# Performance work log

Measured on AMD Instinct MI355X. Metric: run time of the kernel, lower is better.

Reference implementation:

```python
import jax, jax.numpy as jnp
import numpy as np

B, S, P, D = 32, 512, 512, 768

def setup_inputs() -> dict:
    key = jax.random.key(0)
    k1, k2 = jax.random.split(key)
    inputs = jax.random.normal(k1, (B, S, D), dtype=jnp.float32)
    prototypes = jax.random.normal(k2, (P, D), dtype=jnp.float32)
    return {"inputs": inputs, "prototypes": prototypes}

def reference(inputs, prototypes):
    # Squared Euclidean distance from every token vector to every prototype:
    # but the cross term is a GEMM and the huge [B,S,P,D] intermediate is never built).
    x_sq = jnp.sum(inputs * inputs, axis=-1, keepdims=True)          # [B, S, 1]
    p_sq = jnp.sum(prototypes * prototypes, axis=-1)                 # [P]
    cross = jnp.einsum('bsd,pd->bsp', inputs, prototypes)            # [B, S, P]
    distances = x_sq + p_sq[None, None, :] - 2.0 * cross             # [B, S, P]
    return (distances, prototypes)
```

## Files before the change

### kernel.cpp

```cpp
#include <hip/hip_runtime.h>
#include <hip/hip_bf16.h>


#define M_TOK 16384
#define N_PROT 512
#define K_DIM 768

typedef __attribute__((ext_vector_type(4))) float f32x4;
typedef __attribute__((ext_vector_type(8))) short bf16x8;

typedef const __attribute__((address_space(1))) unsigned int g_uint;
typedef __attribute__((address_space(3))) unsigned int l_uint;

__device__ inline unsigned short f2bf(float f) {
    unsigned int u = __float_as_uint(f);
    u += 0x7fffu + ((u >> 16) & 1u);
    return (unsigned short)(u >> 16);
}

__global__ __launch_bounds__(256) void prep_kernel(
    const float* __restrict__ x, const float* __restrict__ p,
    unsigned short* __restrict__ a_bf, unsigned short* __restrict__ b_bf,
    float* __restrict__ x_sq, float* __restrict__ p_sq,
    float* __restrict__ proto_out)
{
    const int row  = blockIdx.x * 4 + (threadIdx.x >> 6);
    const int lane = threadIdx.x & 63;

    const float4* src4;
    unsigned short* dst;
    float4* pout4 = nullptr;
    if (row < M_TOK) {
        src4 = (const float4*)(x + (size_t)row * K_DIM);
        dst  = a_bf + (size_t)row * K_DIM;
    } else {
        const int r = row - M_TOK;
        src4  = (const float4*)(p + (size_t)r * K_DIM);
        dst   = b_bf + (size_t)r * K_DIM;
        pout4 = (float4*)(proto_out + (size_t)r * K_DIM);
    }

    float ssum = 0.0f;
#pragma unroll
    for (int j = 0; j < 3; ++j) {
        const int idx = lane + j * 64;
        float4 v = src4[idx];
        ssum += v.x * v.x + v.y * v.y + v.z * v.z + v.w * v.w;
        ushort4 b;
        b.x = f2bf(v.x); b.y = f2bf(v.y); b.z = f2bf(v.z); b.w = f2bf(v.w);
        ((ushort4*)dst)[idx] = b;
        if (pout4) pout4[idx] = v;
    }

#pragma unroll
    for (int off = 32; off > 0; off >>= 1) ssum += __shfl_down(ssum, off);
    if (lane == 0) {
        if (row < M_TOK) x_sq[row] = ssum;
        else             p_sq[row - M_TOK] = ssum;
    }
}

__global__ __launch_bounds__(256) void gemm_kernel(
    const unsigned short* __restrict__ A,
    const unsigned short* __restrict__ Bt,
    const float* __restrict__ x_sq, const float* __restrict__ p_sq,
    float* __restrict__ out)
{
    __shared__ unsigned short lds_a[128 * 64];
    __shared__ unsigned short lds_b[128 * 64];

    const int tid  = threadIdx.x;
    const int wave = tid >> 6;
    const int lane = tid & 63;
    const int bm = blockIdx.y << 7;
    const int bn = blockIdx.x << 7;
    const int wm = (wave >> 1) << 6;
    const int wn = (wave & 1) << 6;
    const int quad = lane >> 4;
    const int l16  = lane & 15;

    const int srow  = wave * 32;
    const int lrow8 = lane >> 3;
    const int lcol  = (lane & 7) * 8;

    const f32x4 zero = {0.0f, 0.0f, 0.0f, 0.0f};
    f32x4 acc[4][4];
#pragma unroll
    for (int mt = 0; mt < 4; ++mt)
#pragma unroll
        for (int nt = 0; nt < 4; ++nt) acc[mt][nt] = zero;

    for (int k0 = 0; k0 < K_DIM; k0 += 64) {
        __syncthreads();
#pragma unroll
        for (int i = 0; i < 4; ++i) {
            const unsigned short* ga =
                A + (size_t)(bm + srow + i * 8 + lrow8) * K_DIM + k0 + lcol;
            __builtin_amdgcn_global_load_lds((g_uint*)ga,
                (l_uint*)&lds_a[(srow + i * 8) * 64], 16, 0, 0);
            const unsigned short* gb =
                Bt + (size_t)(bn + srow + i * 8 + lrow8) * K_DIM + k0 + lcol;
            __builtin_amdgcn_global_load_lds((g_uint*)gb,
                (l_uint*)&lds_b[(srow + i * 8) * 64], 16, 0, 0);
        }
        __syncthreads();

        bf16x8 af[2][4], bfr[2][4];
#pragma unroll
        for (int ks = 0; ks < 2; ++ks) {
#pragma unroll
            for (int mt = 0; mt < 4; ++mt)
                af[ks][mt] = *(const bf16x8*)
                    &lds_a[(wm + mt * 16 + l16) * 64 + ks * 32 + quad * 8];
#pragma unroll
            for (int nt = 0; nt < 4; ++nt)
                bfr[ks][nt] = *(const bf16x8*)
                    &lds_b[(wn + nt * 16 + l16) * 64 + ks * 32 + quad * 8];
        }

#pragma unroll
        for (int ks = 0; ks < 2; ++ks)
#pragma unroll
            for (int mt = 0; mt < 4; ++mt)
#pragma unroll
                for (int nt = 0; nt < 4; ++nt)
                    acc[mt][nt] = __builtin_amdgcn_mfma_f32_16x16x32_bf16(
                        af[ks][mt], bfr[ks][nt], acc[mt][nt], 0, 0, 0);
    }

    float ps[4];
#pragma unroll
    for (int nt = 0; nt < 4; ++nt) ps[nt] = p_sq[bn + wn + nt * 16 + l16];

#pragma unroll
    for (int mt = 0; mt < 4; ++mt) {
#pragma unroll
        for (int i = 0; i < 4; ++i) {
            const int gr = bm + wm + mt * 16 + quad * 4 + i;
            const float xs = x_sq[gr];
            float* orow = out + (size_t)gr * N_PROT + bn + wn + l16;
#pragma unroll
            for (int nt = 0; nt < 4; ++nt)
                orow[nt * 16] = xs + ps[nt] - 2.0f * acc[mt][nt][i];
        }
    }
}

extern "C" void kernel_launch(void* const* d_in, const int* in_sizes, int n_in,
                              void* d_out, int out_size, void* d_ws, size_t ws_size,
                              hipStream_t stream) {
    const float* inputs = (const float*)d_in[0];
    const float* protos = (const float*)d_in[1];
    float* out = (float*)d_out;

    char* ws = (char*)d_ws;
    unsigned short* a_bf = (unsigned short*)ws;
    unsigned short* b_bf = (unsigned short*)(ws + 25165824);
    float* x_sq = (float*)(ws + 25165824 + 786432);
    float* p_sq = (float*)(ws + 25165824 + 786432 + 65536);
    float* proto_out = out + (size_t)M_TOK * N_PROT;

    prep_kernel<<<4224, 256, 0, stream>>>(inputs, protos, a_bf, b_bf, x_sq, p_sq, proto_out);

    dim3 grid(N_PROT / 128, M_TOK / 128);
    gemm_kernel<<<grid, 256, 0, stream>>>(a_bf, b_bf, x_sq, p_sq, out);
}
```

Measured before the change: 119.2 us.

## Process two rows per wave in prep, remap GEMM block order, add occupancy hint

The prep kernel now has each wave handle two rows and issue all six float4 loads before any compute, so more memory requests are in flight per wave, and it launches half as many blocks. The GEMM switches to a 1D grid where consecutive blocks walk down the M dimension within one N column. This changes which A/B tiles are resident in L2 at the same time. It also adds a launch_bounds minimum of 3 blocks per CU, which may force the compiler to limit registers and could cause spills in the 64-accumulator MFMA loop.

```diff
diff --git a/kernel.cpp b/kernel.cpp
--- a/kernel.cpp
+++ b/kernel.cpp
@@ -24,43 +24,65 @@
     float* __restrict__ x_sq, float* __restrict__ p_sq,
     float* __restrict__ proto_out)
 {
-    const int row  = blockIdx.x * 4 + (threadIdx.x >> 6);
+    const int gw   = blockIdx.x * 4 + (threadIdx.x >> 6);
     const int lane = threadIdx.x & 63;
 
-    const float4* src4;
-    unsigned short* dst;
-    float4* pout4 = nullptr;
-    if (row < M_TOK) {
-        src4 = (const float4*)(x + (size_t)row * K_DIM);
-        dst  = a_bf + (size_t)row * K_DIM;
-    } else {
-        const int r = row - M_TOK;
-        src4  = (const float4*)(p + (size_t)r * K_DIM);
-        dst   = b_bf + (size_t)r * K_DIM;
-        pout4 = (float4*)(proto_out + (size_t)r * K_DIM);
-    }
+    float4 v[2][3];
+    const float4* src4[2];
+    unsigned short* dst[2];
+    float4* pout4[2];
+    int rows[2];
 
-    float ssum = 0.0f;
 #pragma unroll
-    for (int j = 0; j < 3; ++j) {
-        const int idx = lane + j * 64;
-        float4 v = src4[idx];
-        ssum += v.x * v.x + v.y * v.y + v.z * v.z + v.w * v.w;
-        ushort4 b;
-        b.x = f2bf(v.x); b.y = f2bf(v.y); b.z = f2bf(v.z); b.w = f2bf(v.w);
-        ((ushort4*)dst)[idx] = b;
-        if (pout4) pout4[idx] = v;
+    for (int r = 0; r < 2; ++r) {
+        const int row = gw * 2 + r;
+        rows[r] = row;
+        if (row < M_TOK) {
+            src4[r]  = (const float4*)(x + (size_t)row * K_DIM);
+            dst[r]   = a_bf + (size_t)row * K_DIM;
+            pout4[r] = nullptr;
+        } else {
+            const int pr = row - M_TOK;
+            src4[r]  = (const float4*)(p + (size_t)pr * K_DIM);
+            dst[r]   = b_bf + (size_t)pr * K_DIM;
+            pout4[r] = (float4*)(proto_out + (size_t)pr * K_DIM);
+        }
     }
 
 #pragma unroll
-    for (int off = 32; off > 0; off >>= 1) ssum += __shfl_down(ssum, off);
+    for (int r = 0; r < 2; ++r)
+#pragma unroll
+        for (int j = 0; j < 3; ++j)
+            v[r][j] = src4[r][lane + j * 64];
+
+    float ss[2];
+#pragma unroll
+    for (int r = 0; r < 2; ++r) {
+        ss[r] = 0.0f;
+#pragma unroll
+        for (int j = 0; j < 3; ++j) {
+            const int idx = lane + j * 64;
+            float4 w = v[r][j];
+            ss[r] += w.x * w.x + w.y * w.y + w.z * w.z + w.w * w.w;
+            ushort4 b;
+            b.x = f2bf(w.x); b.y = f2bf(w.y); b.z = f2bf(w.z); b.w = f2bf(w.w);
+            ((ushort4*)dst[r])[idx] = b;
+            if (pout4[r]) pout4[r][idx] = w;
+        }
+#pragma unroll
+        for (int off = 32; off > 0; off >>= 1) ss[r] += __shfl_down(ss[r], off);
+    }
+
     if (lane == 0) {
-        if (row < M_TOK) x_sq[row] = ssum;
-        else             p_sq[row - M_TOK] = ssum;
+#pragma unroll
+        for (int r = 0; r < 2; ++r) {
+            if (rows[r] < M_TOK) x_sq[rows[r]] = ss[r];
+            else                 p_sq[rows[r] - M_TOK] = ss[r];
+        }
     }
 }
 
-__global__ __launch_bounds__(256) void gemm_kernel(
+__global__ __launch_bounds__(256, 3) void gemm_kernel(
     const unsigned short* __restrict__ A,
     const unsigned short* __restrict__ Bt,
     const float* __restrict__ x_sq, const float* __restrict__ p_sq,
@@ -72,8 +94,9 @@
     const int tid  = threadIdx.x;
     const int wave = tid >> 6;
     const int lane = tid & 63;
-    const int bm = blockIdx.y << 7;
-    const int bn = blockIdx.x << 7;
+    const int bid  = blockIdx.x;
+    const int bn = (bid >> 7) << 7;
+    const int bm = (bid & 127) << 7;
     const int wm = (wave >> 1) << 6;
     const int wn = (wave & 1) << 6;
     const int quad = lane >> 4;
@@ -160,8 +183,7 @@
     float* p_sq = (float*)(ws + 25165824 + 786432 + 65536);
     float* proto_out = out + (size_t)M_TOK * N_PROT;
 
-    prep_kernel<<<4224, 256, 0, stream>>>(inputs, protos, a_bf, b_bf, x_sq, p_sq, proto_out);
+    prep_kernel<<<2112, 256, 0, stream>>>(inputs, protos, a_bf, b_bf, x_sq, p_sq, proto_out);
 
-    dim3 grid(N_PROT / 128, M_TOK / 128);
-    gemm_kernel<<<grid, 256, 0, stream>>>(a_bf, b_bf, x_sq, p_sq, out);
+    gemm_kernel<<<512, 256, 0, stream>>>(a_bf, b_bf, x_sq, p_sq, out);
 }
```

Result: no change. 117.2 us (-1.7%).
